# Kernel optimization log

Hardware: AMD Instinct MI355X
Metric: run time of the kernel (lower is better)

Reference implementation:

```python
import jax, jax.numpy as jnp
import numpy as np

_Y_PERC = np.array([[0.01840373,0.58999538,0.99887572,1.35731124,1.51378647,1.59615814,1.60794642,1.59768487],[0.54538216,0.85649201,1.15733541,1.48270578,1.60280835,1.63332936,1.6204338,1.60154382],[0.97357237,1.15783744,1.37431718,1.6003753,1.66259869,1.65741183,1.62199538,1.60600917],[1.32983939,1.48646416,1.60701991,1.70982965,1.70294495,1.63899384,1.62378931,1.61771147],[1.51241334,1.61619203,1.6781811,1.69350727,1.68488638,1.62312361,1.60460837,1.59458518],[1.59135561,1.67050663,1.67614207,1.69062219,1.6559363,1.61859251,1.58166148,1.57357605],[1.62406025,1.64713876,1.63513799,1.6238076,1.6050742,1.57471174,1.5501197,1.54399399],[1.6153739,1.60502484,1.59157153,1.58655249,1.57093044,1.56278208,1.54476926,1.52678157]], dtype=np.float32)
_Y_QUANT = np.array([[16,11,10,16,24,40,51,61],[12,12,14,19,26,58,60,55],[14,13,16,24,40,57,69,56],[14,17,22,29,51,87,80,62],[18,22,37,56,68,109,103,77],[24,35,55,64,81,104,113,92],[49,64,78,87,103,121,120,101],[72,92,95,98,112,100,103,99]], dtype=np.float32)

def _dct8_ortho():
    # Orthonormal 8x8 DCT-II matrix (matches T_DCT_ORTHO up to fp32 rounding)
    n = np.arange(8, dtype=np.float64)
    T = np.cos(np.pi * (2.0 * n[None, :] + 1.0) * n[:, None] / 16.0) * np.sqrt(2.0 / 8.0)
    T[0, :] *= np.sqrt(0.5)
    return T.astype(np.float32)

def setup_inputs() -> dict:
    key = jax.random.key(0)
    k1, k2 = jax.random.split(key)
    B, C, H, W = 16, 3, 512, 512
    return {
        "input": jax.random.normal(k1, (B, C, H, W), dtype=jnp.float32),
        "target": jax.random.normal(k2, (B, C, H, W), dtype=jnp.float32),
        "transform": jnp.asarray(_dct8_ortho()),
        "weight": jnp.asarray(_Y_PERC / _Y_QUANT),
    }

def _blocks(x):
    # (B,C,H,W) -> (B,C,nblocks,8,8), same block ordering as torch
    # reshape(B,C,H,W//8,8).transpose(-2,-3).reshape(B,C,-1,8,8)
    B, C, H, W = x.shape
    return x.reshape(B, C, H, W // 8, 8).swapaxes(2, 3).reshape(B, C, -1, 8, 8)

def reference(input, target, transform, weight):
    # Transform is linear, so T@x@T' - T@y@T' == T@(x-y)@T' -- same math, fewer GEMMs.
    diff = _blocks(input) - _blocks(target)
    d = jnp.einsum('ij,bcnjk,lk->bcnil', transform, diff, transform)
    return jnp.mean(d * d * weight)
```

## Files before the change

kernel.cpp:

```cpp
#include <hip/hip_runtime.h>


#define WG 256
#define NWG 768
#define INV_N (1.0f/12582912.0f)

__global__ __launch_bounds__(WG) void spectral_partial(
    const float* __restrict__ x,
    const float* __restrict__ y,
    const float* __restrict__ Tm,
    const float* __restrict__ Wm,
    float* __restrict__ ws)
{
    const int tid = threadIdx.x;
    const int p   = blockIdx.x * WG + tid;
    const int img = p >> 12;
    const int rem = p & 4095;
    const int hb  = rem >> 6;
    const int wb  = rem & 63;
    const int base = img * 262144 + hb * 4096 + wb * 8;

    float tT[8][8];
#pragma unroll
    for (int i = 0; i < 8; ++i) {
        float4 t0 = reinterpret_cast<const float4*>(Tm)[2*i];
        float4 t1 = reinterpret_cast<const float4*>(Tm)[2*i+1];
        tT[i][0]=t0.x; tT[i][1]=t0.y; tT[i][2]=t0.z; tT[i][3]=t0.w;
        tT[i][4]=t1.x; tT[i][5]=t1.y; tT[i][6]=t1.z; tT[i][7]=t1.w;
    }

    float M[8][8];
#pragma unroll
    for (int r = 0; r < 8; ++r) {
        const float4* xp = reinterpret_cast<const float4*>(x + base + r*512);
        const float4* yp = reinterpret_cast<const float4*>(y + base + r*512);
        float4 a0 = xp[0], a1 = xp[1];
        float4 b0 = yp[0], b1 = yp[1];
        float row[8] = {a0.x-b0.x, a0.y-b0.y, a0.z-b0.z, a0.w-b0.w,
                        a1.x-b1.x, a1.y-b1.y, a1.z-b1.z, a1.w-b1.w};
#pragma unroll
        for (int l = 0; l < 8; ++l) {
            float acc = row[0]*tT[l][0];
#pragma unroll
            for (int j = 1; j < 8; ++j) acc += row[j]*tT[l][j];
            M[r][l] = acc;
        }
    }

    float s = 0.0f;
#pragma unroll
    for (int i = 0; i < 8; ++i) {
        float4 w0 = reinterpret_cast<const float4*>(Wm)[2*i];
        float4 w1 = reinterpret_cast<const float4*>(Wm)[2*i+1];
        float wr[8] = {w0.x,w0.y,w0.z,w0.w,w1.x,w1.y,w1.z,w1.w};
#pragma unroll
        for (int l = 0; l < 8; ++l) {
            float d = tT[i][0]*M[0][l];
#pragma unroll
            for (int r = 1; r < 8; ++r) d += tT[i][r]*M[r][l];
            s += wr[l]*d*d;
        }
    }

#pragma unroll
    for (int off = 32; off > 0; off >>= 1) s += __shfl_down(s, off, 64);
    __shared__ float wsum[WG/64];
    if ((tid & 63) == 0) wsum[tid >> 6] = s;
    __syncthreads();
    if (tid == 0) {
        float t = wsum[0];
#pragma unroll
        for (int w = 1; w < WG/64; ++w) t += wsum[w];
        ws[blockIdx.x] = t;
    }
}

__global__ __launch_bounds__(256) void spectral_reduce(
    const float* __restrict__ ws, float* __restrict__ out)
{
    const int tid = threadIdx.x;
    float s = ws[tid] + ws[tid + 256] + ws[tid + 512];
#pragma unroll
    for (int off = 32; off > 0; off >>= 1) s += __shfl_down(s, off, 64);
    __shared__ float wsum[4];
    if ((tid & 63) == 0) wsum[tid >> 6] = s;
    __syncthreads();
    if (tid == 0) out[0] = (wsum[0]+wsum[1]+wsum[2]+wsum[3]) * INV_N;
}

extern "C" void kernel_launch(void* const* d_in, const int* in_sizes, int n_in,
                              void* d_out, int out_size, void* d_ws, size_t ws_size,
                              hipStream_t stream) {
    const float* x  = (const float*)d_in[0];
    const float* y  = (const float*)d_in[1];
    const float* Tm = (const float*)d_in[2];
    const float* Wm = (const float*)d_in[3];
    float* ws  = (float*)d_ws;
    float* out = (float*)d_out;

    spectral_partial<<<NWG, WG, 0, stream>>>(x, y, Tm, Wm, ws);
    spectral_reduce<<<1, 256, 0, stream>>>(ws, out);
}
```

Measured before the change: 25.91 us.

## Split each 8x8 block across two threads and use nontemporal loads

Each DCT block is now handled by two threads, each computing four of the eight output columns, which doubles the thread count and workgroup count and halves per-thread registers and arithmetic. Both threads of a pair still load the full block rows, so global load requests double, though the second load of each pair should hit in cache. Input loads use nontemporal hints, and the final reduction now sums six partials per thread.

```diff
diff --git a/kernel.cpp b/kernel.cpp
--- a/kernel.cpp
+++ b/kernel.cpp
@@ -2,8 +2,10 @@
 
 
 #define WG 256
-#define NWG 768
+#define NWG 1536u
 #define INV_N (1.0f/12582912.0f)
+
+typedef float v4f __attribute__((ext_vector_type(4)));
 
 __global__ __launch_bounds__(WG) void spectral_partial(
     const float* __restrict__ x,
@@ -12,12 +14,14 @@
     const float* __restrict__ Wm,
     float* __restrict__ ws)
 {
-    const int tid = threadIdx.x;
-    const int p   = blockIdx.x * WG + tid;
-    const int img = p >> 12;
-    const int rem = p & 4095;
-    const int hb  = rem >> 6;
-    const int wb  = rem & 63;
+    const int tid  = threadIdx.x;
+    const int gt   = blockIdx.x * WG + tid;
+    const int p    = gt >> 1;
+    const int half = gt & 1;
+    const int img  = p >> 12;
+    const int rem  = p & 4095;
+    const int hb   = rem >> 6;
+    const int wb   = rem & 63;
     const int base = img * 262144 + hb * 4096 + wb * 8;
 
     float tT[8][8];
@@ -28,21 +32,32 @@
         tT[i][0]=t0.x; tT[i][1]=t0.y; tT[i][2]=t0.z; tT[i][3]=t0.w;
         tT[i][4]=t1.x; tT[i][5]=t1.y; tT[i][6]=t1.z; tT[i][7]=t1.w;
     }
+    float tl[4][8];
+#pragma unroll
+    for (int l = 0; l < 4; ++l) {
+        const float* tr = Tm + (half*4 + l)*8;
+        float4 t0 = reinterpret_cast<const float4*>(tr)[0];
+        float4 t1 = reinterpret_cast<const float4*>(tr)[1];
+        tl[l][0]=t0.x; tl[l][1]=t0.y; tl[l][2]=t0.z; tl[l][3]=t0.w;
+        tl[l][4]=t1.x; tl[l][5]=t1.y; tl[l][6]=t1.z; tl[l][7]=t1.w;
+    }
 
-    float M[8][8];
+    float M[8][4];
 #pragma unroll
     for (int r = 0; r < 8; ++r) {
-        const float4* xp = reinterpret_cast<const float4*>(x + base + r*512);
-        const float4* yp = reinterpret_cast<const float4*>(y + base + r*512);
-        float4 a0 = xp[0], a1 = xp[1];
-        float4 b0 = yp[0], b1 = yp[1];
+        const v4f* xp = reinterpret_cast<const v4f*>(x + base + r*512);
+        const v4f* yp = reinterpret_cast<const v4f*>(y + base + r*512);
+        v4f a0 = __builtin_nontemporal_load(xp);
+        v4f a1 = __builtin_nontemporal_load(xp + 1);
+        v4f b0 = __builtin_nontemporal_load(yp);
+        v4f b1 = __builtin_nontemporal_load(yp + 1);
         float row[8] = {a0.x-b0.x, a0.y-b0.y, a0.z-b0.z, a0.w-b0.w,
                         a1.x-b1.x, a1.y-b1.y, a1.z-b1.z, a1.w-b1.w};
 #pragma unroll
-        for (int l = 0; l < 8; ++l) {
-            float acc = row[0]*tT[l][0];
+        for (int l = 0; l < 4; ++l) {
+            float acc = row[0]*tl[l][0];
 #pragma unroll
-            for (int j = 1; j < 8; ++j) acc += row[j]*tT[l][j];
+            for (int j = 1; j < 8; ++j) acc += row[j]*tl[l][j];
             M[r][l] = acc;
         }
     }
@@ -50,11 +65,10 @@
     float s = 0.0f;
 #pragma unroll
     for (int i = 0; i < 8; ++i) {
-        float4 w0 = reinterpret_cast<const float4*>(Wm)[2*i];
-        float4 w1 = reinterpret_cast<const float4*>(Wm)[2*i+1];
-        float wr[8] = {w0.x,w0.y,w0.z,w0.w,w1.x,w1.y,w1.z,w1.w};
+        float4 w4 = *reinterpret_cast<const float4*>(Wm + i*8 + half*4);
+        float wr[4] = {w4.x, w4.y, w4.z, w4.w};
 #pragma unroll
-        for (int l = 0; l < 8; ++l) {
+        for (int l = 0; l < 4; ++l) {
             float d = tT[i][0]*M[0][l];
 #pragma unroll
             for (int r = 1; r < 8; ++r) d += tT[i][r]*M[r][l];
@@ -67,19 +81,16 @@
     __shared__ float wsum[WG/64];
     if ((tid & 63) == 0) wsum[tid >> 6] = s;
     __syncthreads();
-    if (tid == 0) {
-        float t = wsum[0];
-#pragma unroll
-        for (int w = 1; w < WG/64; ++w) t += wsum[w];
-        ws[blockIdx.x] = t;
-    }
+    if (tid == 0) ws[blockIdx.x] = wsum[0] + wsum[1] + wsum[2] + wsum[3];
 }
 
 __global__ __launch_bounds__(256) void spectral_reduce(
     const float* __restrict__ ws, float* __restrict__ out)
 {
     const int tid = threadIdx.x;
-    float s = ws[tid] + ws[tid + 256] + ws[tid + 512];
+    float s = 0.0f;
+#pragma unroll
+    for (int k = 0; k < 6; ++k) s += ws[tid + k*256];
 #pragma unroll
     for (int off = 32; off > 0; off >>= 1) s += __shfl_down(s, off, 64);
     __shared__ float wsum[4];
```

Result: no change. 26.14 us (+0.9%).
